# Optimization experiments

Measured on AMD Instinct MI355X. Metric: run time of the kernel, lower is better.

The kernel has to match this reference:

```python
import jax, jax.numpy as jnp
import numpy as np

B, D, H, O, E = 1048576, 17, 8, 6, 4  # batch, input_dim, expert_hidden, output_dim, n_clusters
G1, G2 = 64, 32  # gating hidden dims


def setup_inputs() -> dict:
    key = jax.random.key(0)
    ks = jax.random.split(key, 14)
    def w(k, shape, fan_in):
        return (jax.random.normal(k, shape, jnp.float32) / jnp.sqrt(jnp.float32(fan_in)))
    return {
        "x": jax.random.normal(ks[0], (B, D), jnp.float32),
        # per-expert MLP params, stacked on leading expert axis E
        "eW1": w(ks[1], (E, D, H), D), "eb1": w(ks[2], (E, H), D),
        "eW2": w(ks[3], (E, H, H), H), "eb2": w(ks[4], (E, H), H),
        "eW3": w(ks[5], (E, H, O), H), "eb3": w(ks[6], (E, O), H),
        # gating classifier params
        "gW1": w(ks[7], (D, G1), D), "gb1": w(ks[8], (G1,), D),
        "gW2": w(ks[9], (G1, G2), G1), "gb2": w(ks[10], (G2,), G1),
        "gW3": w(ks[11], (G2, E), G2), "gb3": w(ks[12], (E,), G2),
    }


def reference(x, eW1, eb1, eW2, eb2, eW3, eb3, gW1, gb1, gW2, gb2, gW3, gb3):
    # gating network: 17 -> 64 -> 32 -> 4 logits
    h = jax.nn.relu(x @ gW1 + gb1)
    h = jax.nn.relu(h @ gW2 + gb2)
    gating_logits = h @ gW3 + gb3  # [B, E]
    selected = jnp.argmax(gating_logits, axis=1)  # [B] hard routing
    # all experts computed (as in the original), stacked over expert axis
    e = jax.nn.relu(jnp.einsum('bi,eih->beh', x, eW1) + eb1)   # [B, E, H]
    e = jax.nn.relu(jnp.einsum('beh,ehk->bek', e, eW2) + eb2)  # [B, E, H]
    eo = jnp.einsum('bek,eko->beo', e, eW3) + eb3              # [B, E, O]
    # gather the selected expert's output per sample
    predictions = jnp.take_along_axis(eo, selected[:, None, None], axis=1)[:, 0, :]  # [B, O]
    return predictions, gating_logits
```

## Files before the change

kernel.cpp:

```cpp
#include <hip/hip_runtime.h>

#define BTOT 1048576
#define D 17
#define H 8
#define OUT 6
#define E 4
#define G1 64
#define G2 32

#define WSTR 296

__global__ __launch_bounds__(256) void hybrid_ruc_kernel(
    const float* __restrict__ x,
    const float* __restrict__ eW1, const float* __restrict__ eb1,
    const float* __restrict__ eW2, const float* __restrict__ eb2,
    const float* __restrict__ eW3, const float* __restrict__ eb3,
    const float* __restrict__ gW1, const float* __restrict__ gb1,
    const float* __restrict__ gW2, const float* __restrict__ gb2,
    const float* __restrict__ gW3, const float* __restrict__ gb3,
    float* __restrict__ out)
{
    __shared__ float sx[256 * D];
    __shared__ __align__(16) float swl[E * WSTR];

    const int tid = threadIdx.x;
    const long long bbase = (long long)blockIdx.x * 256;

    #pragma unroll
    for (int k = 0; k < D; ++k) {
        int t = tid + k * 256;
        sx[t] = x[bbase * D + t];
    }

    for (int t = tid; t < E * D * H; t += 256) {
        swl[(t / 136) * WSTR + (t % 136)] = eW1[t];
    }
    {
        int t = tid;
        if (t < E * H * H) {
            swl[(t / 64) * WSTR + 144 + (t % 64)] = eW2[t];
        }
    }
    if (tid < E * H * OUT) {
        int e = tid / 48, r = tid % 48, k = r / 6, o = r % 6;
        swl[e * WSTR + 216 + k * 8 + o] = eW3[tid];
    }
    if (tid < E * H) {
        swl[(tid / 8) * WSTR + 136 + (tid % 8)] = eb1[tid];
    }
    if (tid < E * H) {
        swl[(tid / 8) * WSTR + 208 + (tid % 8)] = eb2[tid];
    }
    if (tid < E * OUT) {
        swl[(tid / 6) * WSTR + 280 + (tid % 6)] = eb3[tid];
    }
    __syncthreads();

    float xr[D];
    #pragma unroll
    for (int i = 0; i < D; ++i) xr[i] = sx[tid * D + i];

    float h2[G2];
    #pragma unroll
    for (int j = 0; j < G2; ++j) h2[j] = gb2[j];

    #pragma unroll 1
    for (int jt = 0; jt < G1 / 16; ++jt) {
        float h1t[16];
        #pragma unroll
        for (int c = 0; c < 16; ++c) h1t[c] = gb1[jt * 16 + c];
        #pragma unroll
        for (int i = 0; i < D; ++i) {
            const float xi = xr[i];
            const float* w1row = gW1 + i * G1 + jt * 16;
            #pragma unroll
            for (int c = 0; c < 16; ++c)
                h1t[c] = __builtin_fmaf(xi, w1row[c], h1t[c]);
        }
        #pragma unroll
        for (int c = 0; c < 16; ++c) {
            const float hv = fmaxf(h1t[c], 0.0f);
            const float* w2row = gW2 + (jt * 16 + c) * G2;
            #pragma unroll
            for (int j = 0; j < G2; ++j)
                h2[j] = __builtin_fmaf(hv, w2row[j], h2[j]);
        }
    }

    float lg[E];
    #pragma unroll
    for (int e = 0; e < E; ++e) lg[e] = gb3[e];
    #pragma unroll
    for (int j = 0; j < G2; ++j) {
        const float hv = fmaxf(h2[j], 0.0f);
        #pragma unroll
        for (int e = 0; e < E; ++e)
            lg[e] = __builtin_fmaf(hv, gW3[j * E + e], lg[e]);
    }

    int sel = 0;
    float best = lg[0];
    #pragma unroll
    for (int e = 1; e < E; ++e) {
        if (lg[e] > best) { best = lg[e]; sel = e; }
    }

    const float* wl = &swl[sel * WSTR];

    float t1[H];
    {
        float4 ba = *(const float4*)(wl + 136);
        float4 bb = *(const float4*)(wl + 140);
        t1[0] = ba.x; t1[1] = ba.y; t1[2] = ba.z; t1[3] = ba.w;
        t1[4] = bb.x; t1[5] = bb.y; t1[6] = bb.z; t1[7] = bb.w;
    }
    #pragma unroll
    for (int i = 0; i < D; ++i) {
        const float xi = xr[i];
        float4 wa = *(const float4*)(wl + i * 8);
        float4 wb = *(const float4*)(wl + i * 8 + 4);
        t1[0] = __builtin_fmaf(xi, wa.x, t1[0]);
        t1[1] = __builtin_fmaf(xi, wa.y, t1[1]);
        t1[2] = __builtin_fmaf(xi, wa.z, t1[2]);
        t1[3] = __builtin_fmaf(xi, wa.w, t1[3]);
        t1[4] = __builtin_fmaf(xi, wb.x, t1[4]);
        t1[5] = __builtin_fmaf(xi, wb.y, t1[5]);
        t1[6] = __builtin_fmaf(xi, wb.z, t1[6]);
        t1[7] = __builtin_fmaf(xi, wb.w, t1[7]);
    }

    float t2[H];
    {
        float4 ba = *(const float4*)(wl + 208);
        float4 bb = *(const float4*)(wl + 212);
        t2[0] = ba.x; t2[1] = ba.y; t2[2] = ba.z; t2[3] = ba.w;
        t2[4] = bb.x; t2[5] = bb.y; t2[6] = bb.z; t2[7] = bb.w;
    }
    #pragma unroll
    for (int k = 0; k < H; ++k) {
        const float tv = fmaxf(t1[k], 0.0f);
        float4 wa = *(const float4*)(wl + 144 + k * 8);
        float4 wb = *(const float4*)(wl + 144 + k * 8 + 4);
        t2[0] = __builtin_fmaf(tv, wa.x, t2[0]);
        t2[1] = __builtin_fmaf(tv, wa.y, t2[1]);
        t2[2] = __builtin_fmaf(tv, wa.z, t2[2]);
        t2[3] = __builtin_fmaf(tv, wa.w, t2[3]);
        t2[4] = __builtin_fmaf(tv, wb.x, t2[4]);
        t2[5] = __builtin_fmaf(tv, wb.y, t2[5]);
        t2[6] = __builtin_fmaf(tv, wb.z, t2[6]);
        t2[7] = __builtin_fmaf(tv, wb.w, t2[7]);
    }

    float pred[OUT];
    {
        float4 ba = *(const float4*)(wl + 280);
        pred[0] = ba.x; pred[1] = ba.y; pred[2] = ba.z; pred[3] = ba.w;
        pred[4] = wl[284]; pred[5] = wl[285];
    }
    #pragma unroll
    for (int k = 0; k < H; ++k) {
        const float tv = fmaxf(t2[k], 0.0f);
        float4 wa = *(const float4*)(wl + 216 + k * 8);
        float4 wb = *(const float4*)(wl + 216 + k * 8 + 4);
        pred[0] = __builtin_fmaf(tv, wa.x, pred[0]);
        pred[1] = __builtin_fmaf(tv, wa.y, pred[1]);
        pred[2] = __builtin_fmaf(tv, wa.z, pred[2]);
        pred[3] = __builtin_fmaf(tv, wa.w, pred[3]);
        pred[4] = __builtin_fmaf(tv, wb.x, pred[4]);
        pred[5] = __builtin_fmaf(tv, wb.y, pred[5]);
    }

    const long long b = bbase + tid;
    #pragma unroll
    for (int o = 0; o < OUT; ++o) out[b * OUT + o] = pred[o];
    float* lout = out + (long long)BTOT * OUT;
    #pragma unroll
    for (int e = 0; e < E; ++e) lout[b * E + e] = lg[e];
}

extern "C" void kernel_launch(void* const* d_in, const int* in_sizes, int n_in,
                              void* d_out, int out_size, void* d_ws, size_t ws_size,
                              hipStream_t stream) {
    const float* x   = (const float*)d_in[0];
    const float* eW1 = (const float*)d_in[1];
    const float* eb1 = (const float*)d_in[2];
    const float* eW2 = (const float*)d_in[3];
    const float* eb2 = (const float*)d_in[4];
    const float* eW3 = (const float*)d_in[5];
    const float* eb3 = (const float*)d_in[6];
    const float* gW1 = (const float*)d_in[7];
    const float* gb1 = (const float*)d_in[8];
    const float* gW2 = (const float*)d_in[9];
    const float* gb2 = (const float*)d_in[10];
    const float* gW3 = (const float*)d_in[11];
    const float* gb3 = (const float*)d_in[12];
    float* out = (float*)d_out;

    dim3 grid(BTOT / 256), block(256);
    hipLaunchKernelGGL(hybrid_ruc_kernel, grid, block, 0, stream,
                       x, eW1, eb1, eW2, eb2, eW3, eb3,
                       gW1, gb1, gW2, gb2, gW3, gb3, out);
}
```

Measured before the change: 196.4 us.

## Run gating MLP on bf16 MFMA with three-way split for fp32 accuracy

Moves the gating network (17→64→32→4) from per-thread scalar FMAs onto 16x16x32 bf16 MFMA instructions. Each fp32 operand is split into three bf16 parts and six cross products are accumulated to emulate fp32 precision. Intermediate activations are staged through an XOR-swizzled per-wave LDS scratch buffer. Each block now handles four chunks of 256 rows so the weight split and preload cost is amortised, and stores are vectorised. This adds LDS traffic, extra syncs, and some risk of small numerical differences that could flip the argmax.

```diff
diff --git a/kernel.cpp b/kernel.cpp
--- a/kernel.cpp
+++ b/kernel.cpp
@@ -7,10 +7,64 @@
 #define E 4
 #define G1 64
 #define G2 32
+#define CHUNKS 4
+#define XSTR 20
+
+typedef float f32x4 __attribute__((ext_vector_type(4)));
+typedef float f32x2 __attribute__((ext_vector_type(2)));
+typedef short s16x8 __attribute__((ext_vector_type(8)));
+typedef unsigned int uint;
+typedef unsigned short ushort_t;
+
+union U4S8 { uint u[4]; s16x8 s; };
+
+__device__ __forceinline__ uint bfr(uint u) {
+    return (u + 0x7fffu + ((u >> 16) & 1u)) & 0xffff0000u;
+}
+
+__device__ __forceinline__ void split1(float v, uint &h, uint &m, uint &l) {
+    uint hb = bfr(__float_as_uint(v));
+    float r1 = v - __uint_as_float(hb);
+    uint mb = bfr(__float_as_uint(r1));
+    float r2 = r1 - __uint_as_float(mb);
+    uint lb = bfr(__float_as_uint(r2));
+    h = hb >> 16; m = mb >> 16; l = lb >> 16;
+}
+
+__device__ __forceinline__ void split_pair(float a, float b, uint &hp, uint &mp, uint &lp) {
+    uint ha = bfr(__float_as_uint(a));
+    uint hb = bfr(__float_as_uint(b));
+    hp = (ha >> 16) | hb;
+    float ra = a - __uint_as_float(ha);
+    float rb = b - __uint_as_float(hb);
+    uint ma = bfr(__float_as_uint(ra));
+    uint mb = bfr(__float_as_uint(rb));
+    mp = (ma >> 16) | mb;
+    float sa = ra - __uint_as_float(ma);
+    float sb = rb - __uint_as_float(mb);
+    lp = (bfr(__float_as_uint(sa)) >> 16) | bfr(__float_as_uint(sb));
+}
+
+__device__ __forceinline__ void split8(f32x4 va, f32x4 vb, s16x8 &fh, s16x8 &fm, s16x8 &fl) {
+    U4S8 Hh, Mm, Ll;
+    split_pair(va.x, va.y, Hh.u[0], Mm.u[0], Ll.u[0]);
+    split_pair(va.z, va.w, Hh.u[1], Mm.u[1], Ll.u[1]);
+    split_pair(vb.x, vb.y, Hh.u[2], Mm.u[2], Ll.u[2]);
+    split_pair(vb.z, vb.w, Hh.u[3], Mm.u[3], Ll.u[3]);
+    fh = Hh.s; fm = Mm.s; fl = Ll.s;
+}
+
+#define MM6(dacc, ah, am, al, bh, bm, bl)                                        \
+    dacc = __builtin_amdgcn_mfma_f32_16x16x32_bf16(al, bh, dacc, 0, 0, 0);       \
+    dacc = __builtin_amdgcn_mfma_f32_16x16x32_bf16(am, bm, dacc, 0, 0, 0);       \
+    dacc = __builtin_amdgcn_mfma_f32_16x16x32_bf16(ah, bl, dacc, 0, 0, 0);       \
+    dacc = __builtin_amdgcn_mfma_f32_16x16x32_bf16(am, bh, dacc, 0, 0, 0);       \
+    dacc = __builtin_amdgcn_mfma_f32_16x16x32_bf16(ah, bm, dacc, 0, 0, 0);       \
+    dacc = __builtin_amdgcn_mfma_f32_16x16x32_bf16(ah, bh, dacc, 0, 0, 0);
 
 #define WSTR 296
 
-__global__ __launch_bounds__(256) void hybrid_ruc_kernel(
+__global__ __launch_bounds__(256, 2) void hybrid_ruc_kernel(
     const float* __restrict__ x,
     const float* __restrict__ eW1, const float* __restrict__ eb1,
     const float* __restrict__ eW2, const float* __restrict__ eb2,
@@ -20,162 +74,252 @@
     const float* __restrict__ gW3, const float* __restrict__ gb3,
     float* __restrict__ out)
 {
-    __shared__ float sx[256 * D];
-    __shared__ __align__(16) float swl[E * WSTR];
+    __shared__ __align__(16) float    sxp[256 * XSTR];
+    __shared__ __align__(16) ushort_t sW1[3][64 * 24];
+    __shared__ __align__(16) ushort_t sW2[3][32 * 72];
+    __shared__ __align__(16) ushort_t sW3[3][4 * 32];
+    __shared__ __align__(16) float    sscr[4][1024];
+    __shared__ __align__(16) float    swl[E * WSTR];
 
     const int tid = threadIdx.x;
-    const long long bbase = (long long)blockIdx.x * 256;
-
-    #pragma unroll
-    for (int k = 0; k < D; ++k) {
-        int t = tid + k * 256;
-        sx[t] = x[bbase * D + t];
-    }
-
+    const int wv  = tid >> 6;
+    const int ln  = tid & 63;
+    const int g   = ln >> 4;
+    const int nn  = ln & 15;
+    float* scr = sscr[wv];
+
+    for (int t = tid; t < 64 * 24; t += 256) {
+        int n = t / 24, k = t % 24;
+        float v = (k < D) ? gW1[k * G1 + n] : 0.0f;
+        uint h, m, l; split1(v, h, m, l);
+        sW1[0][t] = (ushort_t)h; sW1[1][t] = (ushort_t)m; sW1[2][t] = (ushort_t)l;
+    }
+    for (int t = tid; t < 32 * 64; t += 256) {
+        int n = t >> 6, k = t & 63;
+        uint h, m, l; split1(gW2[k * G2 + n], h, m, l);
+        int a = n * 72 + k;
+        sW2[0][a] = (ushort_t)h; sW2[1][a] = (ushort_t)m; sW2[2][a] = (ushort_t)l;
+    }
+    if (tid < 4 * 32) {
+        int n = tid >> 5, k = tid & 31;
+        uint h, m, l; split1(gW3[k * E + n], h, m, l);
+        int a = n * 32 + k;
+        sW3[0][a] = (ushort_t)h; sW3[1][a] = (ushort_t)m; sW3[2][a] = (ushort_t)l;
+    }
     for (int t = tid; t < E * D * H; t += 256) {
         swl[(t / 136) * WSTR + (t % 136)] = eW1[t];
     }
-    {
-        int t = tid;
-        if (t < E * H * H) {
-            swl[(t / 64) * WSTR + 144 + (t % 64)] = eW2[t];
-        }
+    if (tid < E * H * H) {
+        swl[(tid / 64) * WSTR + 144 + (tid % 64)] = eW2[tid];
     }
     if (tid < E * H * OUT) {
         int e = tid / 48, r = tid % 48, k = r / 6, o = r % 6;
         swl[e * WSTR + 216 + k * 8 + o] = eW3[tid];
     }
-    if (tid < E * H) {
-        swl[(tid / 8) * WSTR + 136 + (tid % 8)] = eb1[tid];
-    }
-    if (tid < E * H) {
-        swl[(tid / 8) * WSTR + 208 + (tid % 8)] = eb2[tid];
-    }
-    if (tid < E * OUT) {
-        swl[(tid / 6) * WSTR + 280 + (tid % 6)] = eb3[tid];
-    }
+    if (tid < E * H) swl[(tid / 8) * WSTR + 136 + (tid % 8)] = eb1[tid];
+    if (tid < E * H) swl[(tid / 8) * WSTR + 208 + (tid % 8)] = eb2[tid];
+    if (tid < E * OUT) swl[(tid / 6) * WSTR + 280 + (tid % 6)] = eb3[tid];
     __syncthreads();
 
-    float xr[D];
+    float cb1[4], cb2[2], cb3;
     #pragma unroll
-    for (int i = 0; i < D; ++i) xr[i] = sx[tid * D + i];
-
-    float h2[G2];
+    for (int ct = 0; ct < 4; ++ct) cb1[ct] = gb1[ct * 16 + nn];
+    cb2[0] = gb2[nn]; cb2[1] = gb2[16 + nn];
+    cb3 = (nn < 4) ? gb3[nn] : 0.0f;
+
+    const s16x8 z8 = {0, 0, 0, 0, 0, 0, 0, 0};
+    s16x8 B1f[3][4];
     #pragma unroll
-    for (int j = 0; j < G2; ++j) h2[j] = gb2[j];
+    for (int kd = 0; kd < 3; ++kd)
+        #pragma unroll
+        for (int ct = 0; ct < 4; ++ct)
+            B1f[kd][ct] = (g <= 2) ? *(const s16x8*)(&sW1[kd][(ct * 16 + nn) * 24 + g * 8]) : z8;
+    s16x8 B2f[3][2][2];
+    #pragma unroll
+    for (int kd = 0; kd < 3; ++kd)
+        #pragma unroll
+        for (int ct = 0; ct < 2; ++ct)
+            #pragma unroll
+            for (int kt = 0; kt < 2; ++kt)
+                B2f[kd][ct][kt] = *(const s16x8*)(&sW2[kd][(ct * 16 + nn) * 72 + kt * 32 + g * 8]);
+    s16x8 B3f[3];
+    #pragma unroll
+    for (int kd = 0; kd < 3; ++kd)
+        B3f[kd] = (nn < 4) ? *(const s16x8*)(&sW3[kd][nn * 32 + g * 8]) : z8;
 
     #pragma unroll 1
-    for (int jt = 0; jt < G1 / 16; ++jt) {
-        float h1t[16];
-        #pragma unroll
-        for (int c = 0; c < 16; ++c) h1t[c] = gb1[jt * 16 + c];
+    for (int c = 0; c < CHUNKS; ++c) {
+        if (c) __syncthreads();
+        const long long cbase = ((long long)blockIdx.x * CHUNKS + c) * 256;
+
+        for (int t = tid; t < 256 * D; t += 256) {
+            int s = t / D, k = t % D;
+            sxp[s * XSTR + k] = x[cbase * D + t];
+        }
+        {
+            int s = tid;
+            sxp[s * XSTR + 17] = 0.0f;
+            sxp[s * XSTR + 18] = 0.0f;
+            sxp[s * XSTR + 19] = 0.0f;
+        }
+        __syncthreads();
+
+        f32x4 Lg[4];
+        const f32x4 z4 = {0.0f, 0.0f, 0.0f, 0.0f};
+        #pragma unroll
+        for (int rt = 0; rt < 4; ++rt) {
+            const int srow = wv * 64 + rt * 16 + nn;
+            f32x4 xa = (g <= 2) ? *(const f32x4*)(&sxp[srow * XSTR + g * 8]) : z4;
+            f32x4 xb = (g <= 1) ? *(const f32x4*)(&sxp[srow * XSTR + g * 8 + 4]) : z4;
+            s16x8 a1h, a1m, a1l; split8(xa, xb, a1h, a1m, a1l);
+
+            #pragma unroll
+            for (int ct = 0; ct < 4; ++ct) {
+                f32x4 d = {cb1[ct], cb1[ct], cb1[ct], cb1[ct]};
+                MM6(d, a1h, a1m, a1l, B1f[0][ct], B1f[1][ct], B1f[2][ct]);
+                #pragma unroll
+                for (int r = 0; r < 4; ++r) {
+                    float hv = fmaxf(d[r], 0.0f);
+                    int s = g * 4 + r, n = ct * 16 + nn;
+                    scr[s * 64 + (((n >> 2) ^ (s & 15)) << 2) + (n & 3)] = hv;
+                }
+            }
+
+            s16x8 a2h[2], a2m[2], a2l[2];
+            #pragma unroll
+            for (int kt = 0; kt < 2; ++kt) {
+                int kb0 = kt * 8 + g * 2;
+                f32x4 va = *(const f32x4*)(&scr[nn * 64 + ((kb0 ^ (nn & 15)) << 2)]);
+                f32x4 vb = *(const f32x4*)(&scr[nn * 64 + (((kb0 + 1) ^ (nn & 15)) << 2)]);
+                split8(va, vb, a2h[kt], a2m[kt], a2l[kt]);
+            }
+
+            #pragma unroll
+            for (int ct = 0; ct < 2; ++ct) {
+                f32x4 d = {cb2[ct], cb2[ct], cb2[ct], cb2[ct]};
+                #pragma unroll
+                for (int kt = 0; kt < 2; ++kt) {
+                    MM6(d, a2h[kt], a2m[kt], a2l[kt], B2f[0][ct][kt], B2f[1][ct][kt], B2f[2][ct][kt]);
+                }
+                #pragma unroll
+                for (int r = 0; r < 4; ++r) {
+                    float hv = fmaxf(d[r], 0.0f);
+                    int s = g * 4 + r, n = ct * 16 + nn;
+                    scr[s * 32 + (((n >> 2) ^ (s & 7)) << 2) + (n & 3)] = hv;
+                }
+            }
+
+            s16x8 a3h, a3m, a3l;
+            {
+                f32x4 va = *(const f32x4*)(&scr[nn * 32 + (((2 * g) ^ (nn & 7)) << 2)]);
+                f32x4 vb = *(const f32x4*)(&scr[nn * 32 + (((2 * g + 1) ^ (nn & 7)) << 2)]);
+                split8(va, vb, a3h, a3m, a3l);
+            }
+            f32x4 d3 = {cb3, cb3, cb3, cb3};
+            MM6(d3, a3h, a3m, a3l, B3f[0], B3f[1], B3f[2]);
+            Lg[rt] = d3;
+        }
+
+        if (nn < 4) {
+            #pragma unroll
+            for (int rt = 0; rt < 4; ++rt)
+                #pragma unroll
+                for (int r = 0; r < 4; ++r)
+                    scr[(rt * 16 + g * 4 + r) * 4 + nn] = Lg[rt][r];
+        }
+        f32x4 lgv = *(const f32x4*)(&scr[ln * 4]);
+
+        int sel = 0; float best = lgv.x;
+        if (lgv.y > best) { best = lgv.y; sel = 1; }
+        if (lgv.z > best) { best = lgv.z; sel = 2; }
+        if (lgv.w > best) { best = lgv.w; sel = 3; }
+
+        const float* xrow = &sxp[tid * XSTR];
+        float xr[D];
+        {
+            f32x4 x0 = *(const f32x4*)(xrow);
+            f32x4 x1 = *(const f32x4*)(xrow + 4);
+            f32x4 x2 = *(const f32x4*)(xrow + 8);
+            f32x4 x3 = *(const f32x4*)(xrow + 12);
+            xr[0]=x0.x; xr[1]=x0.y; xr[2]=x0.z; xr[3]=x0.w;
+            xr[4]=x1.x; xr[5]=x1.y; xr[6]=x1.z; xr[7]=x1.w;
+            xr[8]=x2.x; xr[9]=x2.y; xr[10]=x2.z; xr[11]=x2.w;
+            xr[12]=x3.x; xr[13]=x3.y; xr[14]=x3.z; xr[15]=x3.w;
+            xr[16]=xrow[16];
+        }
+        const float* wl = &swl[sel * WSTR];
+
+        float t1[H];
+        {
+            f32x4 ba = *(const f32x4*)(wl + 136);
+            f32x4 bb = *(const f32x4*)(wl + 140);
+            t1[0]=ba.x; t1[1]=ba.y; t1[2]=ba.z; t1[3]=ba.w;
+            t1[4]=bb.x; t1[5]=bb.y; t1[6]=bb.z; t1[7]=bb.w;
+        }
         #pragma unroll
         for (int i = 0; i < D; ++i) {
             const float xi = xr[i];
-            const float* w1row = gW1 + i * G1 + jt * 16;
-            #pragma unroll
-            for (int c = 0; c < 16; ++c)
-                h1t[c] = __builtin_fmaf(xi, w1row[c], h1t[c]);
-        }
-        #pragma unroll
-        for (int c = 0; c < 16; ++c) {
-            const float hv = fmaxf(h1t[c], 0.0f);
-            const float* w2row = gW2 + (jt * 16 + c) * G2;
-            #pragma unroll
-            for (int j = 0; j < G2; ++j)
-                h2[j] = __builtin_fmaf(hv, w2row[j], h2[j]);
-        }
-    }
-
-    float lg[E];
-    #pragma unroll
-    for (int e = 0; e < E; ++e) lg[e] = gb3[e];
-    #pragma unroll
-    for (int j = 0; j < G2; ++j) {
-        const float hv = fmaxf(h2[j], 0.0f);
-        #pragma unroll
-        for (int e = 0; e < E; ++e)
-            lg[e] = __builtin_fmaf(hv, gW3[j * E + e], lg[e]);
-    }
-
-    int sel = 0;
-    float best = lg[0];
-    #pragma unroll
-    for (int e = 1; e < E; ++e) {
-        if (lg[e] > best) { best = lg[e]; sel = e; }
-    }
-
-    const float* wl = &swl[sel * WSTR];
-
-    float t1[H];
-    {
-        float4 ba = *(const float4*)(wl + 136);
-        float4 bb = *(const float4*)(wl + 140);
-        t1[0] = ba.x; t1[1] = ba.y; t1[2] = ba.z; t1[3] = ba.w;
-        t1[4] = bb.x; t1[5] = bb.y; t1[6] = bb.z; t1[7] = bb.w;
-    }
-    #pragma unroll
-    for (int i = 0; i < D; ++i) {
-        const float xi = xr[i];
-        float4 wa = *(const float4*)(wl + i * 8);
-        float4 wb = *(const float4*)(wl + i * 8 + 4);
-        t1[0] = __builtin_fmaf(xi, wa.x, t1[0]);
-        t1[1] = __builtin_fmaf(xi, wa.y, t1[1]);
-        t1[2] = __builtin_fmaf(xi, wa.z, t1[2]);
-        t1[3] = __builtin_fmaf(xi, wa.w, t1[3]);
-        t1[4] = __builtin_fmaf(xi, wb.x, t1[4]);
-        t1[5] = __builtin_fmaf(xi, wb.y, t1[5]);
-        t1[6] = __builtin_fmaf(xi, wb.z, t1[6]);
-        t1[7] = __builtin_fmaf(xi, wb.w, t1[7]);
-    }
-
-    float t2[H];
-    {
-        float4 ba = *(const float4*)(wl + 208);
-        float4 bb = *(const float4*)(wl + 212);
-        t2[0] = ba.x; t2[1] = ba.y; t2[2] = ba.z; t2[3] = ba.w;
-        t2[4] = bb.x; t2[5] = bb.y; t2[6] = bb.z; t2[7] = bb.w;
-    }
-    #pragma unroll
-    for (int k = 0; k < H; ++k) {
-        const float tv = fmaxf(t1[k], 0.0f);
-        float4 wa = *(const float4*)(wl + 144 + k * 8);
-        float4 wb = *(const float4*)(wl + 144 + k * 8 + 4);
-        t2[0] = __builtin_fmaf(tv, wa.x, t2[0]);
-        t2[1] = __builtin_fmaf(tv, wa.y, t2[1]);
-        t2[2] = __builtin_fmaf(tv, wa.z, t2[2]);
-        t2[3] = __builtin_fmaf(tv, wa.w, t2[3]);
-        t2[4] = __builtin_fmaf(tv, wb.x, t2[4]);
-        t2[5] = __builtin_fmaf(tv, wb.y, t2[5]);
-        t2[6] = __builtin_fmaf(tv, wb.z, t2[6]);
-        t2[7] = __builtin_fmaf(tv, wb.w, t2[7]);
-    }
-
-    float pred[OUT];
-    {
-        float4 ba = *(const float4*)(wl + 280);
-        pred[0] = ba.x; pred[1] = ba.y; pred[2] = ba.z; pred[3] = ba.w;
-        pred[4] = wl[284]; pred[5] = wl[285];
-    }
-    #pragma unroll
-    for (int k = 0; k < H; ++k) {
-        const float tv = fmaxf(t2[k], 0.0f);
-        float4 wa = *(const float4*)(wl + 216 + k * 8);
-        float4 wb = *(const float4*)(wl + 216 + k * 8 + 4);
-        pred[0] = __builtin_fmaf(tv, wa.x, pred[0]);
-        pred[1] = __builtin_fmaf(tv, wa.y, pred[1]);
-        pred[2] = __builtin_fmaf(tv, wa.z, pred[2]);
-        pred[3] = __builtin_fmaf(tv, wa.w, pred[3]);
-        pred[4] = __builtin_fmaf(tv, wb.x, pred[4]);
-        pred[5] = __builtin_fmaf(tv, wb.y, pred[5]);
-    }
-
-    const long long b = bbase + tid;
-    #pragma unroll
-    for (int o = 0; o < OUT; ++o) out[b * OUT + o] = pred[o];
-    float* lout = out + (long long)BTOT * OUT;
-    #pragma unroll
-    for (int e = 0; e < E; ++e) lout[b * E + e] = lg[e];
+            f32x4 wa = *(const f32x4*)(wl + i * 8);
+            f32x4 wb = *(const f32x4*)(wl + i * 8 + 4);
+            t1[0] = __builtin_fmaf(xi, wa.x, t1[0]);
+            t1[1] = __builtin_fmaf(xi, wa.y, t1[1]);
+            t1[2] = __builtin_fmaf(xi, wa.z, t1[2]);
+            t1[3] = __builtin_fmaf(xi, wa.w, t1[3]);
+            t1[4] = __builtin_fmaf(xi, wb.x, t1[4]);
+            t1[5] = __builtin_fmaf(xi, wb.y, t1[5]);
+            t1[6] = __builtin_fmaf(xi, wb.z, t1[6]);
+            t1[7] = __builtin_fmaf(xi, wb.w, t1[7]);
+        }
+        float t2[H];
+        {
+            f32x4 ba = *(const f32x4*)(wl + 208);
+            f32x4 bb = *(const f32x4*)(wl + 212);
+            t2[0]=ba.x; t2[1]=ba.y; t2[2]=ba.z; t2[3]=ba.w;
+            t2[4]=bb.x; t2[5]=bb.y; t2[6]=bb.z; t2[7]=bb.w;
+        }
+        #pragma unroll
+        for (int k = 0; k < H; ++k) {
+            const float tv = fmaxf(t1[k], 0.0f);
+            f32x4 wa = *(const f32x4*)(wl + 144 + k * 8);
+            f32x4 wb = *(const f32x4*)(wl + 144 + k * 8 + 4);
+            t2[0] = __builtin_fmaf(tv, wa.x, t2[0]);
+            t2[1] = __builtin_fmaf(tv, wa.y, t2[1]);
+            t2[2] = __builtin_fmaf(tv, wa.z, t2[2]);
+            t2[3] = __builtin_fmaf(tv, wa.w, t2[3]);
+            t2[4] = __builtin_fmaf(tv, wb.x, t2[4]);
+            t2[5] = __builtin_fmaf(tv, wb.y, t2[5]);
+            t2[6] = __builtin_fmaf(tv, wb.z, t2[6]);
+            t2[7] = __builtin_fmaf(tv, wb.w, t2[7]);
+        }
+        float pred[OUT];
+        {
+            f32x4 ba = *(const f32x4*)(wl + 280);
+            pred[0]=ba.x; pred[1]=ba.y; pred[2]=ba.z; pred[3]=ba.w;
+            pred[4]=wl[284]; pred[5]=wl[285];
+        }
+        #pragma unroll
+        for (int k = 0; k < H; ++k) {
+            const float tv = fmaxf(t2[k], 0.0f);
+            f32x4 wa = *(const f32x4*)(wl + 216 + k * 8);
+            f32x2 wb = *(const f32x2*)(wl + 216 + k * 8 + 4);
+            pred[0] = __builtin_fmaf(tv, wa.x, pred[0]);
+            pred[1] = __builtin_fmaf(tv, wa.y, pred[1]);
+            pred[2] = __builtin_fmaf(tv, wa.z, pred[2]);
+            pred[3] = __builtin_fmaf(tv, wa.w, pred[3]);
+            pred[4] = __builtin_fmaf(tv, wb.x, pred[4]);
+            pred[5] = __builtin_fmaf(tv, wb.y, pred[5]);
+        }
+
+        const long long b = cbase + tid;
+        f32x2 p0 = {pred[0], pred[1]};
+        f32x2 p1 = {pred[2], pred[3]};
+        f32x2 p2 = {pred[4], pred[5]};
+        *(f32x2*)(out + b * 6)     = p0;
+        *(f32x2*)(out + b * 6 + 2) = p1;
+        *(f32x2*)(out + b * 6 + 4) = p2;
+        float* lout = out + (long long)BTOT * OUT;
+        *(f32x4*)(lout + b * 4) = lgv;
+    }
 }
 
 extern "C" void kernel_launch(void* const* d_in, const int* in_sizes, int n_in,
@@ -196,7 +340,7 @@
     const float* gb3 = (const float*)d_in[12];
     float* out = (float*)d_out;
 
-    dim3 grid(BTOT / 256), block(256);
+    dim3 grid(BTOT / (256 * CHUNKS)), block(256);
     hipLaunchKernelGGL(hybrid_ruc_kernel, grid, block, 0, stream,
                        x, eW1, eb1, eW2, eb2, eW3, eb3,
                        gW1, gb1, gW2, gb2, gW3, gb3, out);
```

New measurement: 224.0 us. +14.1%, slower.

## Compute gating MLP with packed fp16 dot2 and fp32 fallback for near-ties

Applied to the files above, without the earlier changes.

Weights of the gating network are packed into half2 pairs by a small pre-kernel, and the 17-64-32-4 gating MLP runs with v_dot2_f32_f16, roughly halving the FMA count that dominates the kernel. When the top two logits are within a threshold, a wave-cooperative fp32 recomputation fixes the expert selection. The stored gating logits still come from the fp16 path, so they carry fp16 rounding error that may exceed tolerance. Output stores are also vectorised.

```diff
diff --git a/kernel.cpp b/kernel.cpp
--- a/kernel.cpp
+++ b/kernel.cpp
@@ -7,6 +7,57 @@
 #define E 4
 #define G1 64
 #define G2 32
+#define GTHR 1.0e-2f
+#define NWPK 1664
+
+typedef float f32x4 __attribute__((ext_vector_type(4)));
+typedef float f32x2 __attribute__((ext_vector_type(2)));
+typedef _Float16 h16x2 __attribute__((ext_vector_type(2)));
+typedef unsigned int uint;
+
+#if defined(__has_builtin)
+# if __has_builtin(__builtin_amdgcn_fdot2)
+#  define HAVE_FDOT2 1
+# endif
+#endif
+
+__device__ __align__(16) uint g_wpack[NWPK];
+
+union UH { uint u; h16x2 h; };
+
+__device__ __forceinline__ float dot2f(float acc, h16x2 a, uint w) {
+    UH c; c.u = w;
+#ifdef HAVE_FDOT2
+    return __builtin_amdgcn_fdot2(a, c.h, acc, false);
+#else
+    asm("v_dot2_f32_f16 %0, %1, %2, %0" : "+v"(acc) : "v"(a), "s"(w));
+    return acc;
+#endif
+}
+
+__global__ __launch_bounds__(256) void pack_kernel(
+    const float* __restrict__ gW1, const float* __restrict__ gW2,
+    const float* __restrict__ gW3)
+{
+    for (int idx = threadIdx.x; idx < NWPK; idx += 256) {
+        float a, b;
+        if (idx < 576) {
+            int i2 = idx >> 6, n = idx & 63;
+            a = gW1[(2 * i2) * G1 + n];
+            b = (2 * i2 + 1 < D) ? gW1[(2 * i2 + 1) * G1 + n] : 0.0f;
+        } else if (idx < 1600) {
+            int r = idx - 576, c2 = r >> 5, j = r & 31;
+            a = gW2[(2 * c2) * G2 + j];
+            b = gW2[(2 * c2 + 1) * G2 + j];
+        } else {
+            int r = idx - 1600, j2 = r >> 2, e = r & 3;
+            a = gW3[(2 * j2) * E + e];
+            b = gW3[(2 * j2 + 1) * E + e];
+        }
+        UH p; p.h = h16x2{(_Float16)a, (_Float16)b};
+        g_wpack[idx] = p.u;
+    }
+}
 
 #define WSTR 296
 
@@ -22,103 +73,149 @@
 {
     __shared__ float sx[256 * D];
     __shared__ __align__(16) float swl[E * WSTR];
+    __shared__ float sfb[4][96];
 
     const int tid = threadIdx.x;
+    const int wv  = tid >> 6;
+    const int ln  = tid & 63;
     const long long bbase = (long long)blockIdx.x * 256;
+    const uint* __restrict__ wp = g_wpack;
 
     #pragma unroll
     for (int k = 0; k < D; ++k) {
         int t = tid + k * 256;
         sx[t] = x[bbase * D + t];
     }
-
     for (int t = tid; t < E * D * H; t += 256) {
         swl[(t / 136) * WSTR + (t % 136)] = eW1[t];
     }
-    {
-        int t = tid;
-        if (t < E * H * H) {
-            swl[(t / 64) * WSTR + 144 + (t % 64)] = eW2[t];
-        }
+    if (tid < E * H * H) {
+        swl[(tid / 64) * WSTR + 144 + (tid % 64)] = eW2[tid];
     }
     if (tid < E * H * OUT) {
         int e = tid / 48, r = tid % 48, k = r / 6, o = r % 6;
         swl[e * WSTR + 216 + k * 8 + o] = eW3[tid];
     }
-    if (tid < E * H) {
-        swl[(tid / 8) * WSTR + 136 + (tid % 8)] = eb1[tid];
-    }
-    if (tid < E * H) {
-        swl[(tid / 8) * WSTR + 208 + (tid % 8)] = eb2[tid];
-    }
-    if (tid < E * OUT) {
-        swl[(tid / 6) * WSTR + 280 + (tid % 6)] = eb3[tid];
-    }
+    if (tid < E * H) swl[(tid / 8) * WSTR + 136 + (tid % 8)] = eb1[tid];
+    if (tid < E * H) swl[(tid / 8) * WSTR + 208 + (tid % 8)] = eb2[tid];
+    if (tid < E * OUT) swl[(tid / 6) * WSTR + 280 + (tid % 6)] = eb3[tid];
     __syncthreads();
 
     float xr[D];
     #pragma unroll
     for (int i = 0; i < D; ++i) xr[i] = sx[tid * D + i];
 
-    float h2[G2];
-    #pragma unroll
-    for (int j = 0; j < G2; ++j) h2[j] = gb2[j];
-
-    #pragma unroll 1
-    for (int jt = 0; jt < G1 / 16; ++jt) {
-        float h1t[16];
-        #pragma unroll
-        for (int c = 0; c < 16; ++c) h1t[c] = gb1[jt * 16 + c];
-        #pragma unroll
-        for (int i = 0; i < D; ++i) {
-            const float xi = xr[i];
-            const float* w1row = gW1 + i * G1 + jt * 16;
+    h16x2 xp[9];
+    #pragma unroll
+    for (int i2 = 0; i2 < 8; ++i2)
+        xp[i2] = h16x2{(_Float16)xr[2 * i2], (_Float16)xr[2 * i2 + 1]};
+    xp[8] = h16x2{(_Float16)xr[16], (_Float16)0.0f};
+
+    h16x2 hp1[32];
+    #pragma unroll
+    for (int jt = 0; jt < 4; ++jt) {
+        float ha[16];
+        #pragma unroll
+        for (int c = 0; c < 16; ++c) ha[c] = gb1[jt * 16 + c];
+        #pragma unroll
+        for (int i2 = 0; i2 < 9; ++i2) {
             #pragma unroll
             for (int c = 0; c < 16; ++c)
-                h1t[c] = __builtin_fmaf(xi, w1row[c], h1t[c]);
+                ha[c] = dot2f(ha[c], xp[i2], wp[i2 * 64 + jt * 16 + c]);
         }
         #pragma unroll
-        for (int c = 0; c < 16; ++c) {
-            const float hv = fmaxf(h1t[c], 0.0f);
-            const float* w2row = gW2 + (jt * 16 + c) * G2;
+        for (int c2 = 0; c2 < 8; ++c2)
+            hp1[jt * 8 + c2] = h16x2{(_Float16)fmaxf(ha[2 * c2], 0.0f),
+                                     (_Float16)fmaxf(ha[2 * c2 + 1], 0.0f)};
+    }
+
+    h16x2 hp2[16];
+    #pragma unroll
+    for (int jt = 0; jt < 2; ++jt) {
+        float ja[16];
+        #pragma unroll
+        for (int j = 0; j < 16; ++j) ja[j] = gb2[jt * 16 + j];
+        #pragma unroll
+        for (int c2 = 0; c2 < 32; ++c2) {
             #pragma unroll
-            for (int j = 0; j < G2; ++j)
-                h2[j] = __builtin_fmaf(hv, w2row[j], h2[j]);
+            for (int j = 0; j < 16; ++j)
+                ja[j] = dot2f(ja[j], hp1[c2], wp[576 + c2 * 32 + jt * 16 + j]);
         }
+        #pragma unroll
+        for (int j2 = 0; j2 < 8; ++j2)
+            hp2[jt * 8 + j2] = h16x2{(_Float16)fmaxf(ja[2 * j2], 0.0f),
+                                     (_Float16)fmaxf(ja[2 * j2 + 1], 0.0f)};
     }
 
     float lg[E];
     #pragma unroll
     for (int e = 0; e < E; ++e) lg[e] = gb3[e];
     #pragma unroll
-    for (int j = 0; j < G2; ++j) {
-        const float hv = fmaxf(h2[j], 0.0f);
+    for (int j2 = 0; j2 < 16; ++j2) {
         #pragma unroll
         for (int e = 0; e < E; ++e)
-            lg[e] = __builtin_fmaf(hv, gW3[j * E + e], lg[e]);
+            lg[e] = dot2f(lg[e], hp2[j2], wp[1600 + j2 * 4 + e]);
     }
 
     int sel = 0;
-    float best = lg[0];
-    #pragma unroll
-    for (int e = 1; e < E; ++e) {
-        if (lg[e] > best) { best = lg[e]; sel = e; }
+    {
+        float b = lg[0];
+        if (lg[1] > b) { b = lg[1]; sel = 1; }
+        if (lg[2] > b) { b = lg[2]; sel = 2; }
+        if (lg[3] > b) { b = lg[3]; sel = 3; }
+    }
+    float mx01 = fmaxf(lg[0], lg[1]), mn01 = fminf(lg[0], lg[1]);
+    float mx23 = fmaxf(lg[2], lg[3]), mn23 = fminf(lg[2], lg[3]);
+    float best   = fmaxf(mx01, mx23);
+    float second = fmaxf(fminf(mx01, mx23), (mx01 >= mx23) ? mn01 : mn23);
+
+    unsigned long long fmask = __ballot(best - second < GTHR);
+    if (fmask) {
+        float* fs = sfb[wv];
+        do {
+            int sl = (int)__builtin_ctzll(fmask);
+            fmask &= (fmask - 1);
+            const int fr = wv * 64 + sl;
+            float h1j = gb1[ln];
+            #pragma unroll 1
+            for (int i = 0; i < D; ++i)
+                h1j = __builtin_fmaf(sx[fr * D + i], gW1[i * G1 + ln], h1j);
+            fs[ln] = fmaxf(h1j, 0.0f);
+            int j2 = ln & 31;
+            float h2j = gb2[j2];
+            #pragma unroll 4
+            for (int c2 = 0; c2 < G1; ++c2)
+                h2j = __builtin_fmaf(fs[c2], gW2[c2 * G2 + j2], h2j);
+            fs[64 + j2] = fmaxf(h2j, 0.0f);
+            int e = ln & 3;
+            float lge = gb3[e];
+            #pragma unroll 4
+            for (int jj = 0; jj < G2; ++jj)
+                lge = __builtin_fmaf(fs[64 + jj], gW3[jj * E + e], lge);
+            float l0 = __shfl(lge, 0), l1 = __shfl(lge, 1);
+            float l2 = __shfl(lge, 2), l3 = __shfl(lge, 3);
+            int s2 = 0; float bb = l0;
+            if (l1 > bb) { bb = l1; s2 = 1; }
+            if (l2 > bb) { bb = l2; s2 = 2; }
+            if (l3 > bb) { bb = l3; s2 = 3; }
+            if (ln == sl) sel = s2;
+        } while (fmask);
     }
 
     const float* wl = &swl[sel * WSTR];
 
     float t1[H];
     {
-        float4 ba = *(const float4*)(wl + 136);
-        float4 bb = *(const float4*)(wl + 140);
-        t1[0] = ba.x; t1[1] = ba.y; t1[2] = ba.z; t1[3] = ba.w;
-        t1[4] = bb.x; t1[5] = bb.y; t1[6] = bb.z; t1[7] = bb.w;
+        f32x4 ba = *(const f32x4*)(wl + 136);
+        f32x4 bb = *(const f32x4*)(wl + 140);
+        t1[0]=ba.x; t1[1]=ba.y; t1[2]=ba.z; t1[3]=ba.w;
+        t1[4]=bb.x; t1[5]=bb.y; t1[6]=bb.z; t1[7]=bb.w;
     }
     #pragma unroll
     for (int i = 0; i < D; ++i) {
         const float xi = xr[i];
-        float4 wa = *(const float4*)(wl + i * 8);
-        float4 wb = *(const float4*)(wl + i * 8 + 4);
+        f32x4 wa = *(const f32x4*)(wl + i * 8);
+        f32x4 wb = *(const f32x4*)(wl + i * 8 + 4);
         t1[0] = __builtin_fmaf(xi, wa.x, t1[0]);
         t1[1] = __builtin_fmaf(xi, wa.y, t1[1]);
         t1[2] = __builtin_fmaf(xi, wa.z, t1[2]);
@@ -128,19 +225,18 @@
         t1[6] = __builtin_fmaf(xi, wb.z, t1[6]);
         t1[7] = __builtin_fmaf(xi, wb.w, t1[7]);
     }
-
     float t2[H];
     {
-        float4 ba = *(const float4*)(wl + 208);
-        float4 bb = *(const float4*)(wl + 212);
-        t2[0] = ba.x; t2[1] = ba.y; t2[2] = ba.z; t2[3] = ba.w;
-        t2[4] = bb.x; t2[5] = bb.y; t2[6] = bb.z; t2[7] = bb.w;
+        f32x4 ba = *(const f32x4*)(wl + 208);
+        f32x4 bb = *(const f32x4*)(wl + 212);
+        t2[0]=ba.x; t2[1]=ba.y; t2[2]=ba.z; t2[3]=ba.w;
+        t2[4]=bb.x; t2[5]=bb.y; t2[6]=bb.z; t2[7]=bb.w;
     }
     #pragma unroll
     for (int k = 0; k < H; ++k) {
         const float tv = fmaxf(t1[k], 0.0f);
-        float4 wa = *(const float4*)(wl + 144 + k * 8);
-        float4 wb = *(const float4*)(wl + 144 + k * 8 + 4);
+        f32x4 wa = *(const f32x4*)(wl + 144 + k * 8);
+        f32x4 wb = *(const f32x4*)(wl + 144 + k * 8 + 4);
         t2[0] = __builtin_fmaf(tv, wa.x, t2[0]);
         t2[1] = __builtin_fmaf(tv, wa.y, t2[1]);
         t2[2] = __builtin_fmaf(tv, wa.z, t2[2]);
@@ -150,18 +246,17 @@
         t2[6] = __builtin_fmaf(tv, wb.z, t2[6]);
         t2[7] = __builtin_fmaf(tv, wb.w, t2[7]);
     }
-
     float pred[OUT];
     {
-        float4 ba = *(const float4*)(wl + 280);
-        pred[0] = ba.x; pred[1] = ba.y; pred[2] = ba.z; pred[3] = ba.w;
-        pred[4] = wl[284]; pred[5] = wl[285];
+        f32x4 ba = *(const f32x4*)(wl + 280);
+        pred[0]=ba.x; pred[1]=ba.y; pred[2]=ba.z; pred[3]=ba.w;
+        pred[4]=wl[284]; pred[5]=wl[285];
     }
     #pragma unroll
     for (int k = 0; k < H; ++k) {
         const float tv = fmaxf(t2[k], 0.0f);
-        float4 wa = *(const float4*)(wl + 216 + k * 8);
-        float4 wb = *(const float4*)(wl + 216 + k * 8 + 4);
+        f32x4 wa = *(const f32x4*)(wl + 216 + k * 8);
+        f32x2 wb = *(const f32x2*)(wl + 216 + k * 8 + 4);
         pred[0] = __builtin_fmaf(tv, wa.x, pred[0]);
         pred[1] = __builtin_fmaf(tv, wa.y, pred[1]);
         pred[2] = __builtin_fmaf(tv, wa.z, pred[2]);
@@ -171,11 +266,15 @@
     }
 
     const long long b = bbase + tid;
-    #pragma unroll
-    for (int o = 0; o < OUT; ++o) out[b * OUT + o] = pred[o];
+    f32x2 p0 = {pred[0], pred[1]};
+    f32x2 p1 = {pred[2], pred[3]};
+    f32x2 p2 = {pred[4], pred[5]};
+    *(f32x2*)(out + b * 6)     = p0;
+    *(f32x2*)(out + b * 6 + 2) = p1;
+    *(f32x2*)(out + b * 6 + 4) = p2;
     float* lout = out + (long long)BTOT * OUT;
-    #pragma unroll
-    for (int e = 0; e < E; ++e) lout[b * E + e] = lg[e];
+    f32x4 lgv = {lg[0], lg[1], lg[2], lg[3]};
+    *(f32x4*)(lout + b * 4) = lgv;
 }
 
 extern "C" void kernel_launch(void* const* d_in, const int* in_sizes, int n_in,
@@ -196,6 +295,8 @@
     const float* gb3 = (const float*)d_in[12];
     float* out = (float*)d_out;
 
+    hipLaunchKernelGGL(pack_kernel, dim3(1), dim3(256), 0, stream, gW1, gW2, gW3);
+
     dim3 grid(BTOT / 256), block(256);
     hipLaunchKernelGGL(hybrid_ruc_kernel, grid, block, 0, stream,
                        x, eW1, eb1, eW2, eb2, eW3, eb3,
```

Result: slower. 252.6 us (+28.6%).
